# Performance work log

Hardware: AMD Instinct MI355X
Metric: run time of the kernel (lower is better)

## Reference

```python
import jax, jax.numpy as jnp
import numpy as np

N = 100000
E = 1600000
D = 128          # in_feat == hidden_size
L = 3            # hidden layers
EPS = 1e-5       # BatchNorm1d eps


def setup_inputs() -> dict:
    key = jax.random.key(0)
    ks = jax.random.split(key, 12)
    x = jax.random.normal(ks[0], (N, D), dtype=jnp.float32)
    edge_index = jax.random.randint(ks[1], (2, E), 0, N, dtype=jnp.int64)
    s = 1.0 / np.sqrt(D)
    # stacked hidden-layer SAGEConv params: lin_l (neighbor), lin_r (root), bias on lin_l
    Wl = jax.random.uniform(ks[2], (L, D, D), jnp.float32, -s, s)
    Wr = jax.random.uniform(ks[3], (L, D, D), jnp.float32, -s, s)
    b = jax.random.uniform(ks[4], (L, D), jnp.float32, -s, s)
    # batchnorm affine params
    gamma = jnp.ones((L, D), jnp.float32)
    beta = jnp.zeros((L, D), jnp.float32)
    # output SAGEConv: D -> 1
    Wl_out = jax.random.uniform(ks[5], (D, 1), jnp.float32, -s, s)
    Wr_out = jax.random.uniform(ks[6], (D, 1), jnp.float32, -s, s)
    b_out = jax.random.uniform(ks[7], (1,), jnp.float32, -s, s)
    return {"x": x, "edge_index": edge_index, "Wl": Wl, "Wr": Wr, "b": b,
            "gamma": gamma, "beta": beta, "Wl_out": Wl_out, "Wr_out": Wr_out,
            "b_out": b_out}


def _sage(x, src, dst, inv_deg, Wl, Wr, b):
    # gather neighbor features along edges, mean-aggregate at destination
    msg_sum = jax.ops.segment_sum(x[src], dst, num_segments=N)   # [N, F]
    mean = msg_sum * inv_deg                                     # 0 for isolated nodes
    return mean @ Wl + x @ Wr + b


def _batchnorm(x, gamma, beta):
    m = jnp.mean(x, axis=0)
    v = jnp.mean((x - m) ** 2, axis=0)  # biased var, as torch BN uses for normalization
    return gamma * (x - m) * jax.lax.rsqrt(v + EPS) + beta


def reference(x, edge_index, Wl, Wr, b, gamma, beta, Wl_out, Wr_out, b_out):
    src, dst = edge_index[0], edge_index[1]
    deg = jax.ops.segment_sum(jnp.ones((E,), x.dtype), dst, num_segments=N)
    inv_deg = jnp.where(deg > 0, 1.0 / jnp.maximum(deg, 1.0), 0.0)[:, None]
    h = x
    for i in range(L):
        h = _sage(h, src, dst, inv_deg, Wl[i], Wr[i], b[i])
        h = jax.nn.relu(h)
        h = _batchnorm(h, gamma[i], beta[i])
    out = _sage(h, src, dst, inv_deg, Wl_out, Wr_out, b_out)
    return jax.nn.sigmoid(out)  # [N, 1]
```

## Files before the change

kernel.cpp:

```cpp
#include <hip/hip_runtime.h>

typedef unsigned short u16;
typedef unsigned int u32;
typedef unsigned long long u64;

#define GN 100000
#define GE 1600000
#define DCAP 64
#define NRANGE 196
#define NBKT (NRANGE * 8)
#define BCAP 1536

typedef __bf16 bf16x8 __attribute__((ext_vector_type(8)));
typedef float f32x4 __attribute__((ext_vector_type(4)));
typedef float f32x2 __attribute__((ext_vector_type(2)));
typedef u32 u32x4 __attribute__((ext_vector_type(4)));
typedef u32 u32x2 __attribute__((ext_vector_type(2)));

__device__ __forceinline__ float bl(u32 u){ return __uint_as_float(u << 16); }
__device__ __forceinline__ float bh(u32 u){ return __uint_as_float(u & 0xffff0000u); }
__device__ __forceinline__ float bfu(u16 v){ return __uint_as_float(((u32)v) << 16); }
__device__ __forceinline__ u16 f2bf(float f){
    u32 u = __float_as_uint(f);
    u32 r = (u + 0x7fffu + ((u >> 16) & 1u)) >> 16;
    return (u16)r;
}
__device__ __forceinline__ u32 pack2(float a, float b){
    return (u32)f2bf(a) | ((u32)f2bf(b) << 16);
}
__device__ __forceinline__ u32 pk8x4(float a, float b, float c, float d){
    u32 p = (u32)__builtin_amdgcn_cvt_pk_fp8_f32(a, b, 0, false);
    p = (u32)__builtin_amdgcn_cvt_pk_fp8_f32(c, d, p, true);
    return p;
}

__global__ void __launch_bounds__(256) k_init(const int* ei, const u32* xraw,
                                              int* cursor, float* colpart, int* flags,
                                              int* bcur){
    int i = blockIdx.x * 256 + threadIdx.x;
    if (i < GN) cursor[i] = 0;
    if (i < NBKT) bcur[i] = 0;
    if (i < 6144) colpart[i] = 0.f;
    int t = threadIdx.x;
    if (blockIdx.x == 0){
        __shared__ int s_any[4];
        int v = 0;
        #pragma unroll
        for (int j = 0; j < 4; ++j){
            int k = t * 4 + j;
            v |= ei[2 * k * 1000 + 1];
        }
        #pragma unroll
        for (int m = 1; m < 64; m <<= 1) v |= __shfl_xor(v, m);
        if ((t & 63) == 0) s_any[t >> 6] = v;
        __syncthreads();
        if (t == 0){
            int any = s_any[0] | s_any[1] | s_any[2] | s_any[3];
            flags[0] = (any == 0) ? 1 : 0;
        }
    }
    if (blockIdx.x == 1){
        __shared__ int s_cnt[4];
        int cnt = 0;
        #pragma unroll
        for (int j = 0; j < 4; ++j){
            int idx = (t * 4 + j) * 6000 + 3;
            u32 u = xraw[idx];
            int e = (u >> 7) & 0xFF;
            cnt += (e >= 100 && e <= 140) ? 1 : 0;
        }
        #pragma unroll
        for (int m = 1; m < 64; m <<= 1) cnt += __shfl_xor(cnt, m);
        if ((t & 63) == 0) s_cnt[t >> 6] = cnt;
        __syncthreads();
        if (t == 0){
            int tot = s_cnt[0] + s_cnt[1] + s_cnt[2] + s_cnt[3];
            flags[1] = (tot > 512) ? 0 : 1;
        }
    }
}

__global__ void __launch_bounds__(256) k_convx(const void* x, const int* flags,
                                               u16* xb, u32* h8){
    int gid = blockIdx.x * 256 + threadIdx.x;
    if (gid >= GN * 16) return;
    float f0,f1,f2,f3,f4,f5,f6,f7;
    if (flags[1]){
        const u32x4* xf = (const u32x4*)x;
        u32x4 a = __builtin_nontemporal_load(xf + gid * 2);
        u32x4 b = __builtin_nontemporal_load(xf + gid * 2 + 1);
        f0 = __uint_as_float(a.x); f1 = __uint_as_float(a.y);
        f2 = __uint_as_float(a.z); f3 = __uint_as_float(a.w);
        f4 = __uint_as_float(b.x); f5 = __uint_as_float(b.y);
        f6 = __uint_as_float(b.z); f7 = __uint_as_float(b.w);
    } else {
        u32x4 g = __builtin_nontemporal_load((const u32x4*)x + gid);
        f0 = bl(g.x); f1 = bh(g.x); f2 = bl(g.y); f3 = bh(g.y);
        f4 = bl(g.z); f5 = bh(g.z); f6 = bl(g.w); f7 = bh(g.w);
    }
    u32x4 o;
    o.x = pack2(f0, f1); o.y = pack2(f2, f3);
    o.z = pack2(f4, f5); o.w = pack2(f6, f7);
    ((u32x4*)xb)[gid] = o;
    u32x2 e = { pk8x4(f0, f1, f2, f3), pk8x4(f4, f5, f6, f7) };
    ((u32x2*)h8)[gid] = e;
}

__global__ void __launch_bounds__(256) k_tofp8(const u16* h, u32* h8){
    int gid = blockIdx.x * 256 + threadIdx.x;
    if (gid >= GN * 16) return;
    u32x4 g = ((const u32x4*)h)[gid];
    u32x2 e = { pk8x4(bl(g.x), bh(g.x), bl(g.y), bh(g.y)),
                pk8x4(bl(g.z), bh(g.z), bl(g.w), bh(g.w)) };
    ((u32x2*)h8)[gid] = e;
}

#define WOFF_WR    49152
#define WOFF_B     98304
#define WOFF_G     98688
#define WOFF_BE    99072
#define WOFF_WLO   99456
#define WOFF_WRO   99584
#define WOFF_BO    99712
#define WTOT       99713
__global__ void __launch_bounds__(256) k_convw(const void* Wl, const void* Wr, const void* b,
                                               const void* g, const void* be, const void* wlo,
                                               const void* wro, const void* bo,
                                               const int* flags, u16* wbuf, float* biasf){
    int i = blockIdx.x * 256 + threadIdx.x;
    if (i >= WTOT) return;
    const void* s; int k;
    if (i < WOFF_B){
        const void* src = (i < WOFF_WR) ? Wl : Wr;
        int r = (i < WOFF_WR) ? i : i - WOFF_WR;
        int layer = r >> 14, L = r & 16383;
        int kk = ((L >> 10) << 3) | (L & 7);
        int cc = (L >> 3) & 127;
        int si = layer * 16384 + kk * 128 + cc;
        float fv = flags[1] ? ((const float*)src)[si] : bfu(((const u16*)src)[si]);
        wbuf[i] = f2bf(fv);
        return;
    }
    if      (i < WOFF_G  ){ s = b;   k = i - WOFF_B; }
    else if (i < WOFF_BE ){ s = g;   k = i - WOFF_G; }
    else if (i < WOFF_WLO){ s = be;  k = i - WOFF_BE; }
    else if (i < WOFF_WRO){ s = wlo; k = i - WOFF_WLO; }
    else if (i < WOFF_BO ){ s = wro; k = i - WOFF_WRO; }
    else                  { s = bo;  k = 0; }
    float fv = flags[1] ? ((const float*)s)[k] : bfu(((const u16*)s)[k]);
    wbuf[i] = f2bf(fv);
    if (i >= WOFF_B && i < WOFF_B + 384) biasf[i - WOFF_B] = fv;
}

__global__ void __launch_bounds__(256) k_fillA(const int* ei, const int* flags,
                                               int* bcur, u64* pairs){
    __shared__ int cnt[256];
    __shared__ int lofs[256];
    __shared__ int gbase[NRANGE];
    __shared__ int wsum[4];
    __shared__ u64 lp[1024];
    int t = threadIdx.x;
    int lane = t & 63, w = t >> 6;
    int res = blockIdx.x & 7;
    int base = blockIdx.x * 1024;
    int is64 = flags[0];
    cnt[t] = 0;
    __syncthreads();
    int myd[4], mys[4], slot[4], myr[4];
    #pragma unroll
    for (int j = 0; j < 4; ++j){
        int e = base + j * 256 + t;
        if (e < GE){
            int d, s;
            if (is64){ d = __builtin_nontemporal_load(ei + 2 * (GE + e));
                       s = __builtin_nontemporal_load(ei + 2 * e); }
            else     { d = __builtin_nontemporal_load(ei + GE + e);
                       s = __builtin_nontemporal_load(ei + e); }
            myd[j] = d; mys[j] = s; myr[j] = d >> 9;
            slot[j] = atomicAdd(&cnt[myr[j]], 1);
        } else myr[j] = -1;
    }
    __syncthreads();
    int v = cnt[t];
    int sv = v;
    #pragma unroll
    for (int d = 1; d < 64; d <<= 1){
        int u = __shfl_up(sv, d);
        if (lane >= d) sv += u;
    }
    if (lane == 63) wsum[w] = sv;
    __syncthreads();
    int prefix = 0;
    #pragma unroll
    for (int j = 0; j < 4; ++j) if (j < w) prefix += wsum[j];
    lofs[t] = sv + prefix - v;
    if (t < NRANGE && cnt[t] > 0)
        gbase[t] = atomicAdd(&bcur[t * 8 + res], cnt[t]);
    __syncthreads();
    #pragma unroll
    for (int j = 0; j < 4; ++j){
        if (myr[j] >= 0)
            lp[lofs[myr[j]] + slot[j]] = ((u64)(u32)myd[j] << 32) | (u32)mys[j];
    }
    __syncthreads();
    int total = GE - base; if (total > 1024) total = 1024;
    for (int i = t; i < total; i += 256){
        u64 pr = lp[i];
        int r = (int)(pr >> 32) >> 9;
        int g = gbase[r] + (i - lofs[r]);
        if (g < BCAP) pairs[((size_t)(r * 8 + res)) * BCAP + g] = pr;
    }
}

__global__ void __launch_bounds__(256) k_fillB(const int* bcur, const u64* pairs,
                                               int* cursor, int* col){
    int range = blockIdx.x % 200;
    int sub   = blockIdx.x / 200;
    if (range >= NRANGE || sub >= 8) return;
    int bkt = range * 8 + sub;
    int n = bcur[bkt]; if (n > BCAP) n = BCAP;
    const u64* P = pairs + (size_t)bkt * BCAP;
    for (int i = threadIdx.x; i < n; i += 256){
        u64 pr = __builtin_nontemporal_load(P + i);
        int s = (int)(u32)pr, d = (int)(pr >> 32);
        int pos = atomicAdd(&cursor[d], 1);
        if (pos < DCAP) col[d * DCAP + pos] = s;
    }
}

__global__ void __launch_bounds__(64) k_agg(const u32* h8, const int* deg, const int* col,
                                            u16* amean){
    int lane = threadIdx.x;
    int grp = lane >> 4;
    int lg  = lane & 15;
    int node = blockIdx.x * 4 + grp;
    if (node >= GN) return;
    int d = deg[node];
    int cnt = d < DCAP ? d : DCAP;
    const int* nb = col + node * DCAP;
    const u32x2* hrow = (const u32x2*)h8;
    f32x2 A01 = {0.f, 0.f}, A23 = {0.f, 0.f}, A45 = {0.f, 0.f}, A67 = {0.f, 0.f};
    int e = 0;
    #define ACC8(v) { \
        A01 += __builtin_amdgcn_cvt_pk_f32_fp8((v).x, false); \
        A23 += __builtin_amdgcn_cvt_pk_f32_fp8((v).x, true);  \
        A45 += __builtin_amdgcn_cvt_pk_f32_fp8((v).y, false); \
        A67 += __builtin_amdgcn_cvt_pk_f32_fp8((v).y, true); }
    for (; e + 7 < cnt; e += 8){
        u32x2 v0 = hrow[(size_t)nb[e]     * 16 + lg];
        u32x2 v1 = hrow[(size_t)nb[e + 1] * 16 + lg];
        u32x2 v2 = hrow[(size_t)nb[e + 2] * 16 + lg];
        u32x2 v3 = hrow[(size_t)nb[e + 3] * 16 + lg];
        u32x2 v4 = hrow[(size_t)nb[e + 4] * 16 + lg];
        u32x2 v5 = hrow[(size_t)nb[e + 5] * 16 + lg];
        u32x2 v6 = hrow[(size_t)nb[e + 6] * 16 + lg];
        u32x2 v7 = hrow[(size_t)nb[e + 7] * 16 + lg];
        ACC8(v0) ACC8(v1) ACC8(v2) ACC8(v3) ACC8(v4) ACC8(v5) ACC8(v6) ACC8(v7)
    }
    for (; e + 1 < cnt; e += 2){
        u32x2 v0 = hrow[(size_t)nb[e]     * 16 + lg];
        u32x2 v1 = hrow[(size_t)nb[e + 1] * 16 + lg];
        ACC8(v0) ACC8(v1)
    }
    if (e < cnt){
        u32x2 v0 = hrow[(size_t)nb[e] * 16 + lg];
        ACC8(v0)
    }
    #undef ACC8
    float inv = (d > 0) ? 1.f / (float)d : 0.f;
    f32x2 iv = {inv, inv};
    A01 *= iv; A23 *= iv; A45 *= iv; A67 *= iv;
    u32x4 o;
    o.x = pack2(A01.x, A01.y);
    o.y = pack2(A23.x, A23.y);
    o.z = pack2(A45.x, A45.y);
    o.w = pack2(A67.x, A67.y);
    ((u32x4*)amean)[(size_t)node * 16 + lg] = o;
}

__global__ void __launch_bounds__(256, 4) k_gemm(const u16* amean, const u16* hin,
                                                 const u16* Wlp, const u16* Wrp,
                                                 const float* biasf,
                                                 u16* hout, float* colpart){
    __shared__ float sst[256];
    int t = threadIdx.x;
    int wid = t >> 6, lane = t & 63;
    int quad = lane >> 4, l15 = lane & 15;
    int r0 = blockIdx.x * 128 + wid * 32;
    int node0 = r0 + l15, node1 = r0 + 16 + l15;
    sst[t] = 0.f;

    f32x4 acc[2][8];
    #pragma unroll
    for (int i = 0; i < 2; i++)
        #pragma unroll
        for (int j = 0; j < 8; j++) acc[i][j] = (f32x4){0.f, 0.f, 0.f, 0.f};

    #pragma unroll
    for (int half = 0; half < 2; ++half){
        const u16* A = half ? hin : amean;
        const u32x4* Wg = (const u32x4*)(half ? Wrp : Wlp);
        #pragma unroll
        for (int s = 0; s < 4; ++s){
            int kk = (s << 5) + (quad << 3);
            union { u32x4 u; bf16x8 v; } fa0, fa1;
            fa0.u = (node0 < GN) ? *(const u32x4*)(A + node0 * 128 + kk) : (u32x4){0,0,0,0};
            fa1.u = (node1 < GN) ? *(const u32x4*)(A + node1 * 128 + kk) : (u32x4){0,0,0,0};
            int kc = (s << 2) + quad;
            const u32x4* wg = Wg + (kc << 7) + l15;
            #pragma unroll
            for (int cb = 0; cb < 8; ++cb){
                union { u32x4 u; bf16x8 v; } fw;
                fw.u = wg[cb << 4];
                acc[0][cb] = __builtin_amdgcn_mfma_f32_16x16x32_bf16(fa0.v, fw.v, acc[0][cb], 0, 0, 0);
                acc[1][cb] = __builtin_amdgcn_mfma_f32_16x16x32_bf16(fa1.v, fw.v, acc[1][cb], 0, 0, 0);
            }
        }
    }
    __syncthreads();

    float bsv[8];
    #pragma unroll
    for (int cb = 0; cb < 8; cb++) bsv[cb] = biasf[cb * 16 + l15];

    #pragma unroll
    for (int cb = 0; cb < 8; cb++){
        float csum = 0.f, csq = 0.f;
        #pragma unroll
        for (int rb = 0; rb < 2; rb++){
            int rbase = r0 + rb * 16 + quad * 4;
            #pragma unroll
            for (int rr = 0; rr < 4; rr++){
                int row = rbase + rr;
                float v = acc[rb][cb][rr] + bsv[cb];
                v = fmaxf(v, 0.f);
                if (row < GN) hout[row * 128 + cb * 16 + l15] = f2bf(v);
                float vm = (row < GN) ? v : 0.f;
                csum += vm; csq += vm * vm;
            }
        }
        csum += __shfl_xor(csum, 16); csum += __shfl_xor(csum, 32);
        csq  += __shfl_xor(csq, 16);  csq  += __shfl_xor(csq, 32);
        if (quad == 0){
            atomicAdd(&sst[cb * 16 + l15], csum);
            atomicAdd(&sst[128 + cb * 16 + l15], csq);
        }
    }
    __syncthreads();
    atomicAdd(&colpart[(blockIdx.x & 7) * 256 + t], sst[t]);
}

__global__ void __launch_bounds__(256) k_bnf(const float* colpart, const u16* gamma, const u16* beta,
                                             int mode,
                                             const u16* WlN, const u16* WrN, u16* wfd,
                                             const float* bNsrc, float* bNdst,
                                             const u16* wlo, const u16* wro, const u16* bo,
                                             u16* hwl, u16* hwr, float* hb){
    __shared__ float s_sc[128], s_sh[128], s_red[256];
    int t = threadIdx.x, b = blockIdx.x;
    if (t < 128){
        float s = 0.f, q = 0.f;
        #pragma unroll
        for (int j = 0; j < 8; ++j){
            s += colpart[j * 256 + t];
            q += colpart[j * 256 + 128 + t];
        }
        const float invn = 1.f / (float)GN;
        float mean = s * invn;
        float var = fmaxf(q * invn - mean * mean, 0.f);
        float rstd = rsqrtf(var + 1e-5f);
        float g  = bfu(gamma[t]);
        float be = bfu(beta[t]);
        float sc = g * rstd, sh = be - mean * sc;
        s_sc[t] = sc; s_sh[t] = sh;
    }
    __syncthreads();
    if (mode == 0){
        if (b < 64){
            int idx = b * 256 + t;
            int k = ((idx >> 10) << 3) | (idx & 7);
            float sc = s_sc[k];
            wfd[idx]         = f2bf(sc * bfu(WlN[idx]));
            wfd[16384 + idx] = f2bf(sc * bfu(WrN[idx]));
        } else if (t < 128){
            float acc = bNsrc[t];
            for (int k = 0; k < 128; ++k){
                int L = ((k >> 3) << 10) + (t << 3) + (k & 7);
                acc += s_sh[k] * (bfu(WlN[L]) + bfu(WrN[L]));
            }
            bNdst[t] = acc;
        }
    } else if (b == 64){
        float contrib = 0.f;
        if (t < 128){
            float wl = bfu(wlo[t]), wr = bfu(wro[t]);
            hwl[t] = f2bf(s_sc[t] * wl);
            hwr[t] = f2bf(s_sc[t] * wr);
            contrib = s_sh[t] * (wl + wr);
        }
        s_red[t] = contrib;
        __syncthreads();
        for (int off = 128; off >= 1; off >>= 1){
            if (t < off) s_red[t] += s_red[t + off];
            __syncthreads();
        }
        if (t == 0) hb[0] = s_red[0] + bfu(bo[0]);
    }
}

__global__ void __launch_bounds__(256) k_dot(const u16* h, const u16* wl, const u16* wr,
                                             float* y, float* r){
    int node = (blockIdx.x * 256 + threadIdx.x) >> 6;
    int lane = threadIdx.x & 63;
    if (node >= GN) return;
    u32 hv  = ((const u32*)h)[node * 64 + lane];
    u32 wlv = ((const u32*)wl)[lane];
    u32 wrv = ((const u32*)wr)[lane];
    float hlo = bl(hv), hhi = bh(hv);
    float ya = hlo * bl(wlv) + hhi * bh(wlv);
    float ra = hlo * bl(wrv) + hhi * bh(wrv);
    #pragma unroll
    for (int m = 1; m < 64; m <<= 1){ ya += __shfl_xor(ya, m); ra += __shfl_xor(ra, m); }
    if (lane == 0){ y[node] = ya; r[node] = ra; }
}

__global__ void __launch_bounds__(256) k_out(const float* y, const float* r, const int* deg,
                                             const int* col, const float* hb,
                                             const int* flags, void* out){
    int n = blockIdx.x * 256 + threadIdx.x;
    if (n >= GN) return;
    int d = deg[n];
    int cnt = d < DCAP ? d : DCAP;
    const int* nb = col + n * DCAP;
    float s = 0.f;
    for (int e = 0; e < cnt; ++e) s += y[nb[e]];
    float inv = (d > 0) ? 1.f / (float)d : 0.f;
    float z = inv * s + r[n] + hb[0];
    float sg = 1.f / (1.f + __expf(-z));
    if (flags[1]) ((float*)out)[n] = sg;
    else          ((u16*)out)[n] = f2bf(sg);
}

extern "C" void kernel_launch(void* const* d_in, const int* in_sizes, int n_in,
                              void* d_out, int out_size, void* d_ws, size_t ws_size,
                              hipStream_t stream) {
    const void* x     = d_in[0];
    const int*  ei    = (const int*)d_in[1];
    const void* Wl    = d_in[2];
    const void* Wr    = d_in[3];
    const void* bias  = d_in[4];
    const void* gamma = d_in[5];
    const void* beta  = d_in[6];
    const void* wlout = d_in[7];
    const void* wrout = d_in[8];
    const void* bout  = d_in[9];

    char* p = (char*)d_ws;
    auto take = [&](size_t b){ void* q = (void*)p; p += (b + 255) & ~(size_t)255; return q; };
    int*   cursor = (int*)  take((size_t)GN * 4);
    int*   flags  = (int*)  take(256);
    int*   bcur   = (int*)  take((size_t)NBKT * 4);
    float* colpart= (float*)take(6144 * 4);
    float* biasf  = (float*)take(384 * 4);
    float* bf2    = (float*)take(128 * 4);
    float* bf3    = (float*)take(128 * 4);
    float* hb     = (float*)take(256);
    u16*   wf2    = (u16*)  take(32768 * 2);
    u16*   wf3    = (u16*)  take(32768 * 2);
    u16*   hwl    = (u16*)  take(128 * 2);
    u16*   hwr    = (u16*)  take(128 * 2);
    float* yv     = (float*)take((size_t)GN * 4);
    float* rv     = (float*)take((size_t)GN * 4);
    int*   col    = (int*)  take((size_t)GN * DCAP * 4);
    u16*   xb     = (u16*)  take((size_t)GN * 128 * 2);
    u16*   amean  = (u16*)  take((size_t)GN * 128 * 2);
    u16*   hbuf   = (u16*)  take((size_t)GN * 128 * 2);
    u32*   h8     = (u32*)  take((size_t)GN * 128);
    u16*   wbuf   = (u16*)  take((size_t)WTOT * 2);

    u64* pairs = (u64*)amean;

    const int NB_N = (GN + 255) / 256;
    const int NB_A4 = (GN + 3) / 4;
    const int NB_W = (GN + 3) / 4;
    const int NB_G = (GN + 127) / 128;
    const int NB_M = (GN * 16 + 255) / 256;
    const int NB_C = (WTOT + 255) / 256;
    const int NB_A = (GE + 1023) / 1024;

    k_init <<<NB_N, 256, 0, stream>>>(ei, (const u32*)x, cursor, colpart, flags, bcur);
    k_convx<<<NB_M, 256, 0, stream>>>(x, flags, xb, h8);
    k_convw<<<NB_C, 256, 0, stream>>>(Wl, Wr, bias, gamma, beta, wlout, wrout, bout, flags, wbuf, biasf);
    k_fillA<<<NB_A, 256, 0, stream>>>(ei, flags, bcur, pairs);
    k_fillB<<<1600, 256, 0, stream>>>(bcur, pairs, cursor, col);

    const u16* hin = xb;
    for (int i = 0; i < 3; ++i){
        const u16* Wlp; const u16* Wrp; const float* bfi;
        if (i == 0){ Wlp = wbuf;     Wrp = wbuf + WOFF_WR; bfi = biasf; }
        else if (i == 1){ Wlp = wf2; Wrp = wf2 + 16384;    bfi = bf2; }
        else { Wlp = wf3;            Wrp = wf3 + 16384;    bfi = bf3; }
        u16* wfd = (i == 0) ? wf2 : wf3;
        float* bNdst = (i == 0) ? bf2 : bf3;
        int nx = (i < 2) ? (i + 1) : 0;
        k_agg <<<NB_A4, 64, 0, stream>>>(h8, cursor, col, amean);
        k_gemm<<<NB_G, 256, 0, stream>>>(amean, hin, Wlp, Wrp, bfi, hbuf,
                                         colpart + i * 2048);
        k_bnf <<<65, 256, 0, stream>>>(colpart + i * 2048,
            wbuf + WOFF_G + i * 128, wbuf + WOFF_BE + i * 128, (i == 2) ? 1 : 0,
            wbuf + nx * 16384, wbuf + WOFF_WR + nx * 16384, wfd,
            biasf + nx * 128, bNdst,
            wbuf + WOFF_WLO, wbuf + WOFF_WRO, wbuf + WOFF_BO, hwl, hwr, hb);
        if (i < 2) k_tofp8<<<NB_M, 256, 0, stream>>>(hbuf, h8);
        hin = hbuf;
    }
    k_dot<<<NB_W, 256, 0, stream>>>(hbuf, hwl, hwr, yv, rv);
    k_out<<<NB_N, 256, 0, stream>>>(yv, rv, cursor, col, hb, flags, d_out);
}
```

Baseline: 447.8 us.

## Fuse neighbor aggregation into GEMM via LDS and emit fp8 features from GEMM epilogue

The separate aggregation kernel is removed. Each GEMM block now gathers and mean-aggregates its 128 nodes' neighbors from fp8 features into a shared-memory tile, then runs the Wl MFMA directly from LDS. The GEMM epilogue also writes the next layer's fp8 copy, so the tofp8 kernel goes away, with ping-pong h8 buffers and a separate pairs buffer. Feature columns are permuted (strided lane layout in convx, matching Wl weight reorder) so the fp8 row layout lines up with the LDS A-operand. This removes the amean round trip and two launches per layer. In exchange the GEMM carries a heavy irregular gather phase with a 34KB LDS footprint, which can reduce occupancy and latency hiding.

```diff
diff --git a/kernel.cpp b/kernel.cpp
--- a/kernel.cpp
+++ b/kernel.cpp
@@ -10,6 +10,7 @@
 #define NRANGE 196
 #define NBKT (NRANGE * 8)
 #define BCAP 1536
+#define LDA 136
 
 typedef __bf16 bf16x8 __attribute__((ext_vector_type(8)));
 typedef float f32x4 __attribute__((ext_vector_type(4)));
@@ -82,37 +83,24 @@
 
 __global__ void __launch_bounds__(256) k_convx(const void* x, const int* flags,
                                                u16* xb, u32* h8){
-    int gid = blockIdx.x * 256 + threadIdx.x;
-    if (gid >= GN * 16) return;
-    float f0,f1,f2,f3,f4,f5,f6,f7;
+    int tid = blockIdx.x * 256 + threadIdx.x;
+    int node = tid >> 4, l15 = tid & 15;
+    if (node >= GN) return;
+    float f[8];
     if (flags[1]){
-        const u32x4* xf = (const u32x4*)x;
-        u32x4 a = __builtin_nontemporal_load(xf + gid * 2);
-        u32x4 b = __builtin_nontemporal_load(xf + gid * 2 + 1);
-        f0 = __uint_as_float(a.x); f1 = __uint_as_float(a.y);
-        f2 = __uint_as_float(a.z); f3 = __uint_as_float(a.w);
-        f4 = __uint_as_float(b.x); f5 = __uint_as_float(b.y);
-        f6 = __uint_as_float(b.z); f7 = __uint_as_float(b.w);
+        const float* xf = (const float*)x + node * 128 + l15;
+        #pragma unroll
+        for (int a = 0; a < 8; ++a) f[a] = __builtin_nontemporal_load(xf + a * 16);
     } else {
-        u32x4 g = __builtin_nontemporal_load((const u32x4*)x + gid);
-        f0 = bl(g.x); f1 = bh(g.x); f2 = bl(g.y); f3 = bh(g.y);
-        f4 = bl(g.z); f5 = bh(g.z); f6 = bl(g.w); f7 = bh(g.w);
-    }
-    u32x4 o;
-    o.x = pack2(f0, f1); o.y = pack2(f2, f3);
-    o.z = pack2(f4, f5); o.w = pack2(f6, f7);
-    ((u32x4*)xb)[gid] = o;
-    u32x2 e = { pk8x4(f0, f1, f2, f3), pk8x4(f4, f5, f6, f7) };
-    ((u32x2*)h8)[gid] = e;
-}
-
-__global__ void __launch_bounds__(256) k_tofp8(const u16* h, u32* h8){
-    int gid = blockIdx.x * 256 + threadIdx.x;
-    if (gid >= GN * 16) return;
-    u32x4 g = ((const u32x4*)h)[gid];
-    u32x2 e = { pk8x4(bl(g.x), bh(g.x), bl(g.y), bh(g.y)),
-                pk8x4(bl(g.z), bh(g.z), bl(g.w), bh(g.w)) };
-    ((u32x2*)h8)[gid] = e;
+        const u16* xh = (const u16*)x + node * 128 + l15;
+        #pragma unroll
+        for (int a = 0; a < 8; ++a) f[a] = bfu(xh[a * 16]);
+    }
+    u16* xo = xb + node * 128 + l15;
+    #pragma unroll
+    for (int a = 0; a < 8; ++a) xo[a * 16] = f2bf(f[a]);
+    u32x2 e = { pk8x4(f[0], f[1], f[2], f[3]), pk8x4(f[4], f[5], f[6], f[7]) };
+    ((u32x2*)h8)[node * 16 + l15] = e;
 }
 
 #define WOFF_WR    49152
@@ -131,10 +119,12 @@
     if (i >= WTOT) return;
     const void* s; int k;
     if (i < WOFF_B){
-        const void* src = (i < WOFF_WR) ? Wl : Wr;
-        int r = (i < WOFF_WR) ? i : i - WOFF_WR;
+        bool isWl = (i < WOFF_WR);
+        const void* src = isWl ? Wl : Wr;
+        int r = isWl ? i : i - WOFF_WR;
         int layer = r >> 14, L = r & 16383;
-        int kk = ((L >> 10) << 3) | (L & 7);
+        int kk = isWl ? (((L & 7) << 4) | (L >> 10))
+                      : (((L >> 10) << 3) | (L & 7));
         int cc = (L >> 3) & 127;
         int si = layer * 16384 + kk * 128 + cc;
         float fv = flags[1] ? ((const float*)src)[si] : bfu(((const u16*)src)[si]);
@@ -228,84 +218,106 @@
     }
 }
 
-__global__ void __launch_bounds__(64) k_agg(const u32* h8, const int* deg, const int* col,
-                                            u16* amean){
-    int lane = threadIdx.x;
-    int grp = lane >> 4;
-    int lg  = lane & 15;
-    int node = blockIdx.x * 4 + grp;
-    if (node >= GN) return;
-    int d = deg[node];
-    int cnt = d < DCAP ? d : DCAP;
-    const int* nb = col + node * DCAP;
-    const u32x2* hrow = (const u32x2*)h8;
-    f32x2 A01 = {0.f, 0.f}, A23 = {0.f, 0.f}, A45 = {0.f, 0.f}, A67 = {0.f, 0.f};
-    int e = 0;
-    #define ACC8(v) { \
-        A01 += __builtin_amdgcn_cvt_pk_f32_fp8((v).x, false); \
-        A23 += __builtin_amdgcn_cvt_pk_f32_fp8((v).x, true);  \
-        A45 += __builtin_amdgcn_cvt_pk_f32_fp8((v).y, false); \
-        A67 += __builtin_amdgcn_cvt_pk_f32_fp8((v).y, true); }
-    for (; e + 7 < cnt; e += 8){
-        u32x2 v0 = hrow[(size_t)nb[e]     * 16 + lg];
-        u32x2 v1 = hrow[(size_t)nb[e + 1] * 16 + lg];
-        u32x2 v2 = hrow[(size_t)nb[e + 2] * 16 + lg];
-        u32x2 v3 = hrow[(size_t)nb[e + 3] * 16 + lg];
-        u32x2 v4 = hrow[(size_t)nb[e + 4] * 16 + lg];
-        u32x2 v5 = hrow[(size_t)nb[e + 5] * 16 + lg];
-        u32x2 v6 = hrow[(size_t)nb[e + 6] * 16 + lg];
-        u32x2 v7 = hrow[(size_t)nb[e + 7] * 16 + lg];
-        ACC8(v0) ACC8(v1) ACC8(v2) ACC8(v3) ACC8(v4) ACC8(v5) ACC8(v6) ACC8(v7)
-    }
-    for (; e + 1 < cnt; e += 2){
-        u32x2 v0 = hrow[(size_t)nb[e]     * 16 + lg];
-        u32x2 v1 = hrow[(size_t)nb[e + 1] * 16 + lg];
-        ACC8(v0) ACC8(v1)
-    }
-    if (e < cnt){
-        u32x2 v0 = hrow[(size_t)nb[e] * 16 + lg];
-        ACC8(v0)
-    }
-    #undef ACC8
-    float inv = (d > 0) ? 1.f / (float)d : 0.f;
-    f32x2 iv = {inv, inv};
-    A01 *= iv; A23 *= iv; A45 *= iv; A67 *= iv;
-    u32x4 o;
-    o.x = pack2(A01.x, A01.y);
-    o.y = pack2(A23.x, A23.y);
-    o.z = pack2(A45.x, A45.y);
-    o.w = pack2(A67.x, A67.y);
-    ((u32x4*)amean)[(size_t)node * 16 + lg] = o;
-}
-
-__global__ void __launch_bounds__(256, 4) k_gemm(const u16* amean, const u16* hin,
+__global__ void __launch_bounds__(256, 4) k_gemm(const u32* h8, const int* deg, const int* col,
+                                                 const u16* hin,
                                                  const u16* Wlp, const u16* Wrp,
-                                                 const float* biasf,
-                                                 u16* hout, float* colpart){
+                                                 const float* biasf, u16* hout,
+                                                 u32* h8o, int write8, float* colpart){
+    __shared__ u16 smA[128 * LDA];
     __shared__ float sst[256];
     int t = threadIdx.x;
     int wid = t >> 6, lane = t & 63;
     int quad = lane >> 4, l15 = lane & 15;
-    int r0 = blockIdx.x * 128 + wid * 32;
-    int node0 = r0 + l15, node1 = r0 + 16 + l15;
+    int r0 = blockIdx.x * 128;
     sst[t] = 0.f;
 
+    {
+        int g = t >> 4, lg = t & 15;
+        const u32x2* hrow = (const u32x2*)h8;
+        #define ACC8(v) { \
+            A01 += __builtin_amdgcn_cvt_pk_f32_fp8((v).x, false); \
+            A23 += __builtin_amdgcn_cvt_pk_f32_fp8((v).x, true);  \
+            A45 += __builtin_amdgcn_cvt_pk_f32_fp8((v).y, false); \
+            A67 += __builtin_amdgcn_cvt_pk_f32_fp8((v).y, true); }
+        for (int m = 0; m < 8; ++m){
+            int lr = g + (m << 4);
+            int node = r0 + lr;
+            f32x2 A01 = {0.f,0.f}, A23 = {0.f,0.f}, A45 = {0.f,0.f}, A67 = {0.f,0.f};
+            int d = 0;
+            if (node < GN){
+                d = deg[node];
+                int cnt = d < DCAP ? d : DCAP;
+                const int* nb = col + node * DCAP;
+                int e = 0;
+                for (; e + 7 < cnt; e += 8){
+                    u32x2 v0 = hrow[(size_t)nb[e]     * 16 + lg];
+                    u32x2 v1 = hrow[(size_t)nb[e + 1] * 16 + lg];
+                    u32x2 v2 = hrow[(size_t)nb[e + 2] * 16 + lg];
+                    u32x2 v3 = hrow[(size_t)nb[e + 3] * 16 + lg];
+                    u32x2 v4 = hrow[(size_t)nb[e + 4] * 16 + lg];
+                    u32x2 v5 = hrow[(size_t)nb[e + 5] * 16 + lg];
+                    u32x2 v6 = hrow[(size_t)nb[e + 6] * 16 + lg];
+                    u32x2 v7 = hrow[(size_t)nb[e + 7] * 16 + lg];
+                    ACC8(v0) ACC8(v1) ACC8(v2) ACC8(v3) ACC8(v4) ACC8(v5) ACC8(v6) ACC8(v7)
+                }
+                for (; e + 1 < cnt; e += 2){
+                    u32x2 v0 = hrow[(size_t)nb[e]     * 16 + lg];
+                    u32x2 v1 = hrow[(size_t)nb[e + 1] * 16 + lg];
+                    ACC8(v0) ACC8(v1)
+                }
+                if (e < cnt){
+                    u32x2 v0 = hrow[(size_t)nb[e] * 16 + lg];
+                    ACC8(v0)
+                }
+            }
+            float inv = (d > 0) ? 1.f / (float)d : 0.f;
+            f32x2 iv = {inv, inv};
+            A01 *= iv; A23 *= iv; A45 *= iv; A67 *= iv;
+            u32x4 o;
+            o.x = pack2(A01.x, A01.y); o.y = pack2(A23.x, A23.y);
+            o.z = pack2(A45.x, A45.y); o.w = pack2(A67.x, A67.y);
+            *(u32x4*)(smA + lr * LDA + lg * 8) = o;
+        }
+        #undef ACC8
+    }
+    __syncthreads();
+
     f32x4 acc[2][8];
     #pragma unroll
     for (int i = 0; i < 2; i++)
         #pragma unroll
         for (int j = 0; j < 8; j++) acc[i][j] = (f32x4){0.f, 0.f, 0.f, 0.f};
 
-    #pragma unroll
-    for (int half = 0; half < 2; ++half){
-        const u16* A = half ? hin : amean;
-        const u32x4* Wg = (const u32x4*)(half ? Wrp : Wlp);
+    int node0 = r0 + wid * 32 + l15, node1 = node0 + 16;
+
+    {
+        const u32x4* Wg = (const u32x4*)Wlp;
+        const u16* a0 = smA + (wid * 32 + l15) * LDA;
+        const u16* a1 = a0 + 16 * LDA;
+        #pragma unroll
+        for (int s = 0; s < 4; ++s){
+            int kc = (s << 2) + quad;
+            union { u32x4 u; bf16x8 v; } fa0, fa1;
+            fa0.u = *(const u32x4*)(a0 + (kc << 3));
+            fa1.u = *(const u32x4*)(a1 + (kc << 3));
+            const u32x4* wg = Wg + (kc << 7) + l15;
+            #pragma unroll
+            for (int cb = 0; cb < 8; ++cb){
+                union { u32x4 u; bf16x8 v; } fw;
+                fw.u = wg[cb << 4];
+                acc[0][cb] = __builtin_amdgcn_mfma_f32_16x16x32_bf16(fa0.v, fw.v, acc[0][cb], 0, 0, 0);
+                acc[1][cb] = __builtin_amdgcn_mfma_f32_16x16x32_bf16(fa1.v, fw.v, acc[1][cb], 0, 0, 0);
+            }
+        }
+    }
+    {
+        const u32x4* Wg = (const u32x4*)Wrp;
         #pragma unroll
         for (int s = 0; s < 4; ++s){
             int kk = (s << 5) + (quad << 3);
             union { u32x4 u; bf16x8 v; } fa0, fa1;
-            fa0.u = (node0 < GN) ? *(const u32x4*)(A + node0 * 128 + kk) : (u32x4){0,0,0,0};
-            fa1.u = (node1 < GN) ? *(const u32x4*)(A + node1 * 128 + kk) : (u32x4){0,0,0,0};
+            fa0.u = (node0 < GN) ? *(const u32x4*)(hin + node0 * 128 + kk) : (u32x4){0,0,0,0};
+            fa1.u = (node1 < GN) ? *(const u32x4*)(hin + node1 * 128 + kk) : (u32x4){0,0,0,0};
             int kc = (s << 2) + quad;
             const u32x4* wg = Wg + (kc << 7) + l15;
             #pragma unroll
@@ -317,33 +329,44 @@
             }
         }
     }
-    __syncthreads();
 
     float bsv[8];
     #pragma unroll
     for (int cb = 0; cb < 8; cb++) bsv[cb] = biasf[cb * 16 + l15];
-
+    float csum[8], csq[8];
+    #pragma unroll
+    for (int cb = 0; cb < 8; cb++){ csum[cb] = 0.f; csq[cb] = 0.f; }
+
+    #pragma unroll
+    for (int rb = 0; rb < 2; ++rb){
+        #pragma unroll
+        for (int rr = 0; rr < 4; ++rr){
+            int row = r0 + wid * 32 + rb * 16 + quad * 4 + rr;
+            float v[8];
+            #pragma unroll
+            for (int cb = 0; cb < 8; ++cb) v[cb] = fmaxf(acc[rb][cb][rr] + bsv[cb], 0.f);
+            if (row < GN){
+                #pragma unroll
+                for (int cb = 0; cb < 8; ++cb){
+                    hout[row * 128 + cb * 16 + l15] = f2bf(v[cb]);
+                    csum[cb] += v[cb]; csq[cb] += v[cb] * v[cb];
+                }
+                if (write8){
+                    u32x2 pp = { pk8x4(v[0], v[1], v[2], v[3]),
+                                 pk8x4(v[4], v[5], v[6], v[7]) };
+                    ((u32x2*)h8o)[row * 16 + l15] = pp;
+                }
+            }
+        }
+    }
     #pragma unroll
     for (int cb = 0; cb < 8; cb++){
-        float csum = 0.f, csq = 0.f;
-        #pragma unroll
-        for (int rb = 0; rb < 2; rb++){
-            int rbase = r0 + rb * 16 + quad * 4;
-            #pragma unroll
-            for (int rr = 0; rr < 4; rr++){
-                int row = rbase + rr;
-                float v = acc[rb][cb][rr] + bsv[cb];
-                v = fmaxf(v, 0.f);
-                if (row < GN) hout[row * 128 + cb * 16 + l15] = f2bf(v);
-                float vm = (row < GN) ? v : 0.f;
-                csum += vm; csq += vm * vm;
-            }
-        }
-        csum += __shfl_xor(csum, 16); csum += __shfl_xor(csum, 32);
-        csq  += __shfl_xor(csq, 16);  csq  += __shfl_xor(csq, 32);
+        float cs = csum[cb], cq = csq[cb];
+        cs += __shfl_xor(cs, 16); cs += __shfl_xor(cs, 32);
+        cq += __shfl_xor(cq, 16); cq += __shfl_xor(cq, 32);
         if (quad == 0){
-            atomicAdd(&sst[cb * 16 + l15], csum);
-            atomicAdd(&sst[128 + cb * 16 + l15], csq);
+            atomicAdd(&sst[cb * 16 + l15], cs);
+            atomicAdd(&sst[128 + cb * 16 + l15], cq);
         }
     }
     __syncthreads();
@@ -378,15 +401,16 @@
     if (mode == 0){
         if (b < 64){
             int idx = b * 256 + t;
-            int k = ((idx >> 10) << 3) | (idx & 7);
-            float sc = s_sc[k];
-            wfd[idx]         = f2bf(sc * bfu(WlN[idx]));
-            wfd[16384 + idx] = f2bf(sc * bfu(WrN[idx]));
+            int kl = ((idx & 7) << 4) | (idx >> 10);
+            int kr = ((idx >> 10) << 3) | (idx & 7);
+            wfd[idx]         = f2bf(s_sc[kl] * bfu(WlN[idx]));
+            wfd[16384 + idx] = f2bf(s_sc[kr] * bfu(WrN[idx]));
         } else if (t < 128){
             float acc = bNsrc[t];
             for (int k = 0; k < 128; ++k){
-                int L = ((k >> 3) << 10) + (t << 3) + (k & 7);
-                acc += s_sh[k] * (bfu(WlN[L]) + bfu(WrN[L]));
+                int Ll = ((k & 15) << 10) + (t << 3) + (k >> 4);
+                int Lr = ((k >> 3) << 10) + (t << 3) + (k & 7);
+                acc += s_sh[k] * (bfu(WlN[Ll]) + bfu(WrN[Lr]));
             }
             bNdst[t] = acc;
         }
@@ -473,15 +497,13 @@
     float* rv     = (float*)take((size_t)GN * 4);
     int*   col    = (int*)  take((size_t)GN * DCAP * 4);
     u16*   xb     = (u16*)  take((size_t)GN * 128 * 2);
-    u16*   amean  = (u16*)  take((size_t)GN * 128 * 2);
     u16*   hbuf   = (u16*)  take((size_t)GN * 128 * 2);
-    u32*   h8     = (u32*)  take((size_t)GN * 128);
+    u32*   h8a    = (u32*)  take((size_t)GN * 128);
+    u32*   h8b    = (u32*)  take((size_t)GN * 128);
+    u64*   pairs  = (u64*)  take((size_t)NBKT * BCAP * 8);
     u16*   wbuf   = (u16*)  take((size_t)WTOT * 2);
 
-    u64* pairs = (u64*)amean;
-
     const int NB_N = (GN + 255) / 256;
-    const int NB_A4 = (GN + 3) / 4;
     const int NB_W = (GN + 3) / 4;
     const int NB_G = (GN + 127) / 128;
     const int NB_M = (GN * 16 + 255) / 256;
@@ -489,7 +511,7 @@
     const int NB_A = (GE + 1023) / 1024;
 
     k_init <<<NB_N, 256, 0, stream>>>(ei, (const u32*)x, cursor, colpart, flags, bcur);
-    k_convx<<<NB_M, 256, 0, stream>>>(x, flags, xb, h8);
+    k_convx<<<NB_M, 256, 0, stream>>>(x, flags, xb, h8a);
     k_convw<<<NB_C, 256, 0, stream>>>(Wl, Wr, bias, gamma, beta, wlout, wrout, bout, flags, wbuf, biasf);
     k_fillA<<<NB_A, 256, 0, stream>>>(ei, flags, bcur, pairs);
     k_fillB<<<1600, 256, 0, stream>>>(bcur, pairs, cursor, col);
@@ -503,15 +525,16 @@
         u16* wfd = (i == 0) ? wf2 : wf3;
         float* bNdst = (i == 0) ? bf2 : bf3;
         int nx = (i < 2) ? (i + 1) : 0;
-        k_agg <<<NB_A4, 64, 0, stream>>>(h8, cursor, col, amean);
-        k_gemm<<<NB_G, 256, 0, stream>>>(amean, hin, Wlp, Wrp, bfi, hbuf,
+        const u32* h8i = (i == 1) ? h8b : h8a;
+        u32*       h8o = (i == 0) ? h8b : h8a;
+        k_gemm<<<NB_G, 256, 0, stream>>>(h8i, cursor, col, hin, Wlp, Wrp, bfi,
+                                         hbuf, (i == 2) ? h8b : h8o, (i < 2) ? 1 : 0,
                                          colpart + i * 2048);
         k_bnf <<<65, 256, 0, stream>>>(colpart + i * 2048,
             wbuf + WOFF_G + i * 128, wbuf + WOFF_BE + i * 128, (i == 2) ? 1 : 0,
             wbuf + nx * 16384, wbuf + WOFF_WR + nx * 16384, wfd,
             biasf + nx * 128, bNdst,
             wbuf + WOFF_WLO, wbuf + WOFF_WRO, wbuf + WOFF_BO, hwl, hwr, hb);
-        if (i < 2) k_tofp8<<<NB_M, 256, 0, stream>>>(hbuf, h8);
         hin = hbuf;
     }
     k_dot<<<NB_W, 256, 0, stream>>>(hbuf, hwl, hwr, yv, rv);
```

Measured after the change: 459.0 us. 1.03x slower.
